# Optimization experiments

Hardware: AMD Instinct MI355X
Metric: run time of the kernel (lower is better)

The kernel has to match this reference:

```python
import jax, jax.numpy as jnp
import numpy as np

N_NODES = 50000
NODE_DIM = 256
HIDDEN = 512
N_EDGES = 500000


def setup_inputs() -> dict:
    key = jax.random.key(0)
    k1, k2, k3, k4 = jax.random.split(key, 4)
    x = jax.random.normal(k1, (N_NODES, NODE_DIM), dtype=jnp.float32)
    edge_index = jax.random.randint(k2, (2, N_EDGES), 0, N_NODES, dtype=jnp.int64)
    in_dim = 2 * NODE_DIM  # concat mode
    W1 = jax.random.normal(k3, (in_dim, HIDDEN), dtype=jnp.float32) / np.sqrt(in_dim)
    b1 = jnp.zeros((HIDDEN,), dtype=jnp.float32)
    W2 = jax.random.normal(k4, (HIDDEN, 1), dtype=jnp.float32) / np.sqrt(HIDDEN)
    b2 = jnp.zeros((1,), dtype=jnp.float32)
    return {"x": x, "edge_index": edge_index, "W1": W1, "b1": b1, "W2": W2, "b2": b2}


def reference(x, edge_index, W1, b1, W2, b2):
    row, col = edge_index[0], edge_index[1]
    # concat mode: edge_feat [E, 2*node_dim]
    edge_feat = jnp.concatenate([x[row], x[col]], axis=1)
    h = jax.nn.relu(edge_feat @ W1 + b1)  # [E, hidden]
    score = (h @ W2 + b2).squeeze(-1)     # [E]
    return score
```

## Files before the change

### kernel.cpp

```cpp
#include <hip/hip_runtime.h>
#include <hip/hip_bf16.h>

#define N_NODES  50000
#define NODE_DIM 256
#define HIDDEN   512
#define N_EDGES  500000
#define M_PAD    50048
#define NCAT     1024
#define KDIM     256
#define NB       391
#define CAP      1536
#define NSLOTS   (NB * CAP)
#define QSCALE   30.238095f
#define DSCALE   0.033070866f
#define DUMMY    0xFFFFFFFF00000000ULL

typedef __attribute__((ext_vector_type(4))) unsigned short ushort4v;
typedef __attribute__((ext_vector_type(8))) __bf16 bf16x8;
typedef __attribute__((ext_vector_type(4))) float f32x4;
typedef __attribute__((ext_vector_type(4))) unsigned int uint4v;
typedef __attribute__((ext_vector_type(2))) unsigned int uint2v;
typedef __attribute__((ext_vector_type(2))) unsigned long long ull2;
typedef __attribute__((ext_vector_type(2))) float float2v;

__device__ __forceinline__ unsigned short f2bf(float f) {
  unsigned int u = __builtin_bit_cast(unsigned int, f);
  u += 0x7fffu + ((u >> 16) & 1u);
  return (unsigned short)(u >> 16);
}

__device__ __forceinline__ void gload16(const void* g, void* l) {
  __builtin_amdgcn_global_load_lds(
      (__attribute__((address_space(1))) void*)(g),
      (__attribute__((address_space(3))) void*)(l),
      16, 0, 0);
}

__global__ void prep_kernel(const float* __restrict__ x, unsigned short* __restrict__ xb,
                            const float* __restrict__ W1, unsigned short* __restrict__ wt,
                            int* __restrict__ counts, unsigned long long* __restrict__ slots) {
  const int b = blockIdx.x;
  if (b < 2048) {
    const int total4 = M_PAD * NODE_DIM / 4;
    const int valid4 = N_NODES * NODE_DIM / 4;
    for (int i = b * 256 + threadIdx.x; i < total4; i += 2048 * 256) {
      ushort4v o;
      if (i < valid4) {
        float4 v = ((const float4*)x)[i];
        o[0] = f2bf(v.x); o[1] = f2bf(v.y); o[2] = f2bf(v.z); o[3] = f2bf(v.w);
      } else {
        o[0] = 0; o[1] = 0; o[2] = 0; o[3] = 0;
      }
      ((ushort4v*)xb)[i] = o;
    }
  } else if (b < 3072) {
    int i = (b - 2048) * 256 + threadIdx.x;
    int n = i >> 8;
    int k = i & 255;
    int srow = (n >= HIDDEN) ? (NODE_DIM + k) : k;
    int scol = n & (HIDDEN - 1);
    wt[i] = f2bf(W1[srow * HIDDEN + scol]);
  } else if (b == 3072) {
    for (int i = threadIdx.x; i < NB; i += 256) counts[i] = 0;
  } else {
    int bb = b - 3073;
    for (int i = bb * 256 + threadIdx.x; i < NSLOTS; i += 512 * 256)
      slots[i] = DUMMY;
  }
}

__global__ __launch_bounds__(256, 2) void gemm_kernel(
    const unsigned short* __restrict__ Xb,
    const unsigned short* __restrict__ Wt,
    const float* __restrict__ b1,
    unsigned short* __restrict__ CbA,
    signed char* __restrict__ CbB) {
  __shared__ unsigned short As[128 * 32];
  __shared__ unsigned short Bs[128 * 32];
  const int t = threadIdx.x;
  const int w = t >> 6;
  const int lane = t & 63;
  const int bid = blockIdx.x;
  const int xcd = bid & 7;
  const int loc = bid >> 3;
  const int tileN = loc / 49;
  const int tileM = xcd * 49 + (loc - tileN * 49);
  if (tileM >= 391) return;
  const int wm = w >> 1, wn = w & 1;

  f32x4 acc[4][4] = {};

  const int rowA0 = tileM * 128;
  const int rowB0 = tileN * 128;
  const int rstage = t >> 2;
  const int cstage = (t & 3) * 8;

  for (int kk = 0; kk < KDIM; kk += 32) {
#pragma unroll
    for (int i = 0; i < 2; ++i) {
      const unsigned short* srcA = Xb + (size_t)(rowA0 + i * 64 + rstage) * KDIM + kk + cstage;
      gload16(srcA, (char*)As + i * 4096 + w * 1024);
      const unsigned short* srcB = Wt + (size_t)(rowB0 + i * 64 + rstage) * KDIM + kk + cstage;
      gload16(srcB, (char*)Bs + i * 4096 + w * 1024);
    }
    __syncthreads();

    bf16x8 a[4], bfr[4];
#pragma unroll
    for (int fm = 0; fm < 4; ++fm)
      a[fm] = *(const bf16x8*)&As[(wm * 64 + fm * 16 + (lane & 15)) * 32 + (lane >> 4) * 8];
#pragma unroll
    for (int fn = 0; fn < 4; ++fn)
      bfr[fn] = *(const bf16x8*)&Bs[(wn * 64 + fn * 16 + (lane & 15)) * 32 + (lane >> 4) * 8];
#pragma unroll
    for (int fm = 0; fm < 4; ++fm)
#pragma unroll
      for (int fn = 0; fn < 4; ++fn)
        acc[fm][fn] = __builtin_amdgcn_mfma_f32_16x16x32_bf16(a[fm], bfr[fn], acc[fm][fn], 0, 0, 0);
    __syncthreads();
  }

  const int row0 = tileM * 128 + wm * 64;
  if (tileN < 4) {
    const int col0 = tileN * 128 + wn * 64;
    float b1v[4];
#pragma unroll
    for (int fn = 0; fn < 4; ++fn) b1v[fn] = b1[col0 + fn * 16 + (lane & 15)];
#pragma unroll
    for (int fm = 0; fm < 4; ++fm)
#pragma unroll
      for (int fn = 0; fn < 4; ++fn)
#pragma unroll
        for (int r = 0; r < 4; ++r) {
          int row = row0 + fm * 16 + (lane >> 4) * 4 + r;
          int col = col0 + fn * 16 + (lane & 15);
          CbA[(size_t)row * HIDDEN + col] = f2bf(acc[fm][fn][r] + b1v[fn]);
        }
  } else {
    const int col0 = (tileN - 4) * 128 + wn * 64;
#pragma unroll
    for (int fm = 0; fm < 4; ++fm)
#pragma unroll
      for (int fn = 0; fn < 4; ++fn)
#pragma unroll
        for (int r = 0; r < 4; ++r) {
          int row = row0 + fm * 16 + (lane >> 4) * 4 + r;
          int col = col0 + fn * 16 + (lane & 15);
          float v = fminf(fmaxf(acc[fm][fn][r], -4.2f), 4.2f);
          CbB[(size_t)row * HIDDEN + col] = (signed char)__float2int_rn(v * QSCALE);
        }
  }
}

__global__ void scatter_kernel(const int* __restrict__ ei, int* __restrict__ counts,
                               unsigned long long* __restrict__ slots) {
  __shared__ int h[NB];
  __shared__ int bbase[NB];
  const int chunk = (N_EDGES + gridDim.x - 1) / gridDim.x;
  const int e0 = blockIdx.x * chunk;
  const int e1 = min(e0 + chunk, N_EDGES);
  for (int i = threadIdx.x; i < NB; i += blockDim.x) h[i] = 0;
  __syncthreads();
  for (int e = e0 + threadIdx.x; e < e1; e += blockDim.x)
    atomicAdd(&h[ei[e] >> 7], 1);
  __syncthreads();
  for (int i = threadIdx.x; i < NB; i += blockDim.x) {
    int c = h[i];
    bbase[i] = c ? atomicAdd(&counts[i], c) : 0;
    h[i] = 0;
  }
  __syncthreads();
  for (int e = e0 + threadIdx.x; e < e1; e += blockDim.x) {
    int r = ei[e];
    int c = ei[N_EDGES + e];
    int b = r >> 7;
    int idx = bbase[b] + atomicAdd(&h[b], 1);
    slots[(size_t)b * CAP + idx] =
        (unsigned long long)r | ((unsigned long long)c << 16) | ((unsigned long long)e << 32);
  }
}

__device__ __forceinline__ float2v edge_mlp_pk(uint4v ua, uint2v ub,
                                               const float2v* w2p) {
  const float2v dscale2 = {DSCALE, DSCALE};
  const float2v zero2 = {0.f, 0.f};
  float2v acc = zero2;
#pragma unroll
  for (int j = 0; j < 4; ++j) {
    unsigned int au = ua[j];
    float2v a;
    a[0] = __builtin_bit_cast(float, au << 16);
    a[1] = __builtin_bit_cast(float, au & 0xffff0000u);
    unsigned int ubw = ub[j >> 1];
    int sh = (j & 1) * 16;
    float2v q;
    q[0] = (float)(int)(signed char)(ubw >> sh);
    q[1] = (float)(int)(signed char)(ubw >> (sh + 8));
    float2v h = __builtin_elementwise_fma(q, dscale2, a);
    h = __builtin_elementwise_max(h, zero2);
    acc = __builtin_elementwise_fma(h, w2p[j], acc);
  }
  return acc;
}

__global__ __launch_bounds__(256) void edge_kernel(
    const unsigned short* __restrict__ CbA,
    const signed char* __restrict__ CbB,
    const unsigned long long* __restrict__ slots,
    const float* __restrict__ W2,
    const float* __restrict__ b2,
    float* __restrict__ out) {
  const int lane = threadIdx.x & 63;
  const int xcd = blockIdx.x & 7;
  const int lwid = (blockIdx.x >> 3) * 4 + (threadIdx.x >> 6);
  const int nlw = (gridDim.x >> 3) * 4;
  const int per_xcd = NSLOTS / 8;
  const int pbase = xcd * per_xcd;
  const int base = lane * 8;

  float2v w2p[4];
  {
    float4 u0 = *(const float4*)&W2[base];
    float4 u1 = *(const float4*)&W2[base + 4];
    w2p[0] = (float2v){u0.x, u0.y};
    w2p[1] = (float2v){u0.z, u0.w};
    w2p[2] = (float2v){u1.x, u1.y};
    w2p[3] = (float2v){u1.z, u1.w};
  }
  const float bias2 = b2[0];

  const int pend = pbase + per_xcd;
  for (int p = pbase + lwid * 2; p < pend; p += nlw * 2) {
    ull2 rr = *(const ull2*)(slots + p);
    const int id0 = (int)(rr[0] >> 32);
    const int id1 = (int)(rr[1] >> 32);
    if ((id0 & id1) < 0) continue;
    const int r0 = (int)(rr[0] & 0xFFFF), c0 = (int)((rr[0] >> 16) & 0xFFFF);
    const int r1 = (int)(rr[1] & 0xFFFF), c1 = (int)((rr[1] >> 16) & 0xFFFF);
    uint4v ua0 = *(const uint4v*)(CbA + (size_t)r0 * HIDDEN + base);
    uint2v ub0 = *(const uint2v*)(CbB + (size_t)c0 * HIDDEN + base);
    uint4v ua1 = *(const uint4v*)(CbA + (size_t)r1 * HIDDEN + base);
    uint2v ub1 = *(const uint2v*)(CbB + (size_t)c1 * HIDDEN + base);

    float2v a0 = edge_mlp_pk(ua0, ub0, w2p);
    float2v a1 = edge_mlp_pk(ua1, ub1, w2p);
    float acc0 = a0[0] + a0[1];
    float acc1 = a1[0] + a1[1];
#pragma unroll
    for (int off = 32; off; off >>= 1) {
      acc0 += __shfl_xor(acc0, off, 64);
      acc1 += __shfl_xor(acc1, off, 64);
    }
    if (lane == 0) {
      if (id0 >= 0) out[id0] = acc0 + bias2;
      if (id1 >= 0) out[id1] = acc1 + bias2;
    }
  }
}

extern "C" void kernel_launch(void* const* d_in, const int* in_sizes, int n_in,
                              void* d_out, int out_size, void* d_ws, size_t ws_size,
                              hipStream_t stream) {
  const float* x  = (const float*)d_in[0];
  const int*   ei = (const int*)d_in[1];
  const float* W1 = (const float*)d_in[2];
  const float* b1 = (const float*)d_in[3];
  const float* W2 = (const float*)d_in[4];
  const float* b2 = (const float*)d_in[5];
  float* out = (float*)d_out;

  char* ws = (char*)d_ws;
  const size_t xb_bytes  = (size_t)M_PAD * KDIM * 2;
  const size_t wt_bytes  = (size_t)NCAT * KDIM * 2;
  const size_t cbA_bytes = (size_t)M_PAD * HIDDEN * 2;
  const size_t cbB_bytes = (size_t)M_PAD * HIDDEN;
  unsigned short* xb  = (unsigned short*)ws;
  unsigned short* wt  = (unsigned short*)(ws + xb_bytes);
  unsigned short* cbA = (unsigned short*)(ws + xb_bytes + wt_bytes);
  signed char*    cbB = (signed char*)(ws + xb_bytes + wt_bytes + cbA_bytes);
  char* tail = ws + xb_bytes + wt_bytes + cbA_bytes + cbB_bytes;
  int* counts = (int*)tail;
  unsigned long long* slots = (unsigned long long*)(tail + 4096);

  hipLaunchKernelGGL(prep_kernel, dim3(3585), dim3(256), 0, stream, x, xb, W1, wt, counts, slots);
  hipLaunchKernelGGL(gemm_kernel, dim3(392 * 8), dim3(256), 0, stream,
                     xb, wt, b1, cbA, cbB);
  hipLaunchKernelGGL(scatter_kernel, dim3(512), dim3(256), 0, stream, ei, counts, slots);
  hipLaunchKernelGGL(edge_kernel, dim3(2048), dim3(256), 0, stream, cbA, cbB, slots, W2, b2, out);
}
```

Baseline: 151.8 us.

## Replace bucketed edge slots with per-row CSR sort and row-reuse edge loop

Replaces the coarse 128-row bucket slots (padded with dummy records) with an exact CSR layout built from a per-source-node histogram, a three-kernel prefix scan, and an atomic-cursor scatter. The edge kernel now iterates over source rows, loading and unpacking each row's CbA slice once and reusing it for all of that row's edges, so only CbB is gathered per edge. This removes the dummy-slot fill and per-edge CbA gathers, but adds four small kernel launches and per-node global atomics. Per-row work is uneven, which may cause load imbalance across waves.

```diff
diff --git a/kernel.cpp b/kernel.cpp
--- a/kernel.cpp
+++ b/kernel.cpp
@@ -8,19 +8,15 @@
 #define M_PAD    50048
 #define NCAT     1024
 #define KDIM     256
-#define NB       391
-#define CAP      1536
-#define NSLOTS   (NB * CAP)
+#define NROWF    50176
 #define QSCALE   30.238095f
 #define DSCALE   0.033070866f
-#define DUMMY    0xFFFFFFFF00000000ULL
 
 typedef __attribute__((ext_vector_type(4))) unsigned short ushort4v;
 typedef __attribute__((ext_vector_type(8))) __bf16 bf16x8;
 typedef __attribute__((ext_vector_type(4))) float f32x4;
 typedef __attribute__((ext_vector_type(4))) unsigned int uint4v;
 typedef __attribute__((ext_vector_type(2))) unsigned int uint2v;
-typedef __attribute__((ext_vector_type(2))) unsigned long long ull2;
 typedef __attribute__((ext_vector_type(2))) float float2v;
 
 __device__ __forceinline__ unsigned short f2bf(float f) {
@@ -38,7 +34,7 @@
 
 __global__ void prep_kernel(const float* __restrict__ x, unsigned short* __restrict__ xb,
                             const float* __restrict__ W1, unsigned short* __restrict__ wt,
-                            int* __restrict__ counts, unsigned long long* __restrict__ slots) {
+                            int* __restrict__ hist) {
   const int b = blockIdx.x;
   if (b < 2048) {
     const int total4 = M_PAD * NODE_DIM / 4;
@@ -60,12 +56,9 @@
     int srow = (n >= HIDDEN) ? (NODE_DIM + k) : k;
     int scol = n & (HIDDEN - 1);
     wt[i] = f2bf(W1[srow * HIDDEN + scol]);
-  } else if (b == 3072) {
-    for (int i = threadIdx.x; i < NB; i += 256) counts[i] = 0;
   } else {
-    int bb = b - 3073;
-    for (int i = bb * 256 + threadIdx.x; i < NSLOTS; i += 512 * 256)
-      slots[i] = DUMMY;
+    for (int i = (b - 3072) * 256 + threadIdx.x; i < NROWF; i += 513 * 256)
+      hist[i] = 0;
   }
 }
 
@@ -152,70 +145,81 @@
   }
 }
 
-__global__ void scatter_kernel(const int* __restrict__ ei, int* __restrict__ counts,
-                               unsigned long long* __restrict__ slots) {
-  __shared__ int h[NB];
-  __shared__ int bbase[NB];
-  const int chunk = (N_EDGES + gridDim.x - 1) / gridDim.x;
-  const int e0 = blockIdx.x * chunk;
-  const int e1 = min(e0 + chunk, N_EDGES);
-  for (int i = threadIdx.x; i < NB; i += blockDim.x) h[i] = 0;
+__global__ void hist_kernel(const int* __restrict__ ei, int* __restrict__ hist) {
+  for (int e = blockIdx.x * 256 + threadIdx.x; e < N_EDGES; e += gridDim.x * 256)
+    atomicAdd(&hist[ei[e]], 1);
+}
+
+__global__ void scanA_kernel(const int* __restrict__ hist, int* __restrict__ psum) {
+  __shared__ int s[256];
+  const int t = threadIdx.x;
+  s[t] = hist[blockIdx.x * 256 + t];
   __syncthreads();
-  for (int e = e0 + threadIdx.x; e < e1; e += blockDim.x)
-    atomicAdd(&h[ei[e] >> 7], 1);
+  for (int o = 128; o; o >>= 1) {
+    if (t < o) s[t] += s[t + o];
+    __syncthreads();
+  }
+  if (t == 0) psum[blockIdx.x] = s[0];
+}
+
+__global__ void scanB_kernel(const int* __restrict__ psum, int* __restrict__ pbase) {
+  __shared__ int s[256];
+  const int t = threadIdx.x;
+  int v = (t < 196) ? psum[t] : 0;
+  s[t] = v;
   __syncthreads();
-  for (int i = threadIdx.x; i < NB; i += blockDim.x) {
-    int c = h[i];
-    bbase[i] = c ? atomicAdd(&counts[i], c) : 0;
-    h[i] = 0;
-  }
+  for (int o = 1; o < 256; o <<= 1) {
+    int u = (t >= o) ? s[t - o] : 0;
+    __syncthreads();
+    s[t] += u;
+    __syncthreads();
+  }
+  if (t < 196) pbase[t] = s[t] - v;
+}
+
+__global__ void scanC_kernel(const int* __restrict__ hist, const int* __restrict__ pbase,
+                             int* __restrict__ offs, int* __restrict__ cursor) {
+  __shared__ int s[256];
+  const int t = threadIdx.x;
+  const int idx = blockIdx.x * 256 + t;
+  int v = hist[idx];
+  s[t] = v;
   __syncthreads();
-  for (int e = e0 + threadIdx.x; e < e1; e += blockDim.x) {
+  for (int o = 1; o < 256; o <<= 1) {
+    int u = (t >= o) ? s[t - o] : 0;
+    __syncthreads();
+    s[t] += u;
+    __syncthreads();
+  }
+  int off = pbase[blockIdx.x] + s[t] - v;
+  offs[idx] = off;
+  cursor[idx] = off;
+}
+
+__global__ void scatter_kernel(const int* __restrict__ ei, int* __restrict__ cursor,
+                               unsigned long long* __restrict__ recs) {
+  for (int e = blockIdx.x * 256 + threadIdx.x; e < N_EDGES; e += gridDim.x * 256) {
     int r = ei[e];
     int c = ei[N_EDGES + e];
-    int b = r >> 7;
-    int idx = bbase[b] + atomicAdd(&h[b], 1);
-    slots[(size_t)b * CAP + idx] =
-        (unsigned long long)r | ((unsigned long long)c << 16) | ((unsigned long long)e << 32);
-  }
-}
-
-__device__ __forceinline__ float2v edge_mlp_pk(uint4v ua, uint2v ub,
-                                               const float2v* w2p) {
-  const float2v dscale2 = {DSCALE, DSCALE};
-  const float2v zero2 = {0.f, 0.f};
-  float2v acc = zero2;
-#pragma unroll
-  for (int j = 0; j < 4; ++j) {
-    unsigned int au = ua[j];
-    float2v a;
-    a[0] = __builtin_bit_cast(float, au << 16);
-    a[1] = __builtin_bit_cast(float, au & 0xffff0000u);
-    unsigned int ubw = ub[j >> 1];
-    int sh = (j & 1) * 16;
-    float2v q;
-    q[0] = (float)(int)(signed char)(ubw >> sh);
-    q[1] = (float)(int)(signed char)(ubw >> (sh + 8));
-    float2v h = __builtin_elementwise_fma(q, dscale2, a);
-    h = __builtin_elementwise_max(h, zero2);
-    acc = __builtin_elementwise_fma(h, w2p[j], acc);
-  }
-  return acc;
+    int pos = atomicAdd(&cursor[r], 1);
+    recs[pos] = (unsigned long long)(unsigned int)c | ((unsigned long long)e << 32);
+  }
 }
 
 __global__ __launch_bounds__(256) void edge_kernel(
     const unsigned short* __restrict__ CbA,
     const signed char* __restrict__ CbB,
-    const unsigned long long* __restrict__ slots,
+    const int* __restrict__ offs,
+    const unsigned long long* __restrict__ recs,
     const float* __restrict__ W2,
     const float* __restrict__ b2,
     float* __restrict__ out) {
   const int lane = threadIdx.x & 63;
   const int xcd = blockIdx.x & 7;
-  const int lwid = (blockIdx.x >> 3) * 4 + (threadIdx.x >> 6);
+  const int lw = (blockIdx.x >> 3) * 4 + (threadIdx.x >> 6);
   const int nlw = (gridDim.x >> 3) * 4;
-  const int per_xcd = NSLOTS / 8;
-  const int pbase = xcd * per_xcd;
+  const int ROWS_X = NROWF / 8;
+  const int rbase = xcd * ROWS_X;
   const int base = lane * 8;
 
   float2v w2p[4];
@@ -228,32 +232,84 @@
     w2p[3] = (float2v){u1.z, u1.w};
   }
   const float bias2 = b2[0];
-
-  const int pend = pbase + per_xcd;
-  for (int p = pbase + lwid * 2; p < pend; p += nlw * 2) {
-    ull2 rr = *(const ull2*)(slots + p);
-    const int id0 = (int)(rr[0] >> 32);
-    const int id1 = (int)(rr[1] >> 32);
-    if ((id0 & id1) < 0) continue;
-    const int r0 = (int)(rr[0] & 0xFFFF), c0 = (int)((rr[0] >> 16) & 0xFFFF);
-    const int r1 = (int)(rr[1] & 0xFFFF), c1 = (int)((rr[1] >> 16) & 0xFFFF);
-    uint4v ua0 = *(const uint4v*)(CbA + (size_t)r0 * HIDDEN + base);
-    uint2v ub0 = *(const uint2v*)(CbB + (size_t)c0 * HIDDEN + base);
-    uint4v ua1 = *(const uint4v*)(CbA + (size_t)r1 * HIDDEN + base);
-    uint2v ub1 = *(const uint2v*)(CbB + (size_t)c1 * HIDDEN + base);
-
-    float2v a0 = edge_mlp_pk(ua0, ub0, w2p);
-    float2v a1 = edge_mlp_pk(ua1, ub1, w2p);
-    float acc0 = a0[0] + a0[1];
-    float acc1 = a1[0] + a1[1];
-#pragma unroll
-    for (int off = 32; off; off >>= 1) {
-      acc0 += __shfl_xor(acc0, off, 64);
-      acc1 += __shfl_xor(acc1, off, 64);
-    }
-    if (lane == 0) {
-      if (id0 >= 0) out[id0] = acc0 + bias2;
-      if (id1 >= 0) out[id1] = acc1 + bias2;
+  const float2v dscale2 = {DSCALE, DSCALE};
+  const float2v zero2 = {0.f, 0.f};
+
+  for (int r = rbase + lw; r < rbase + ROWS_X; r += nlw) {
+    if (r >= N_NODES) continue;
+    const int off0 = offs[r];
+    const int off1 = offs[r + 1];
+    if (off0 == off1) continue;
+
+    uint4v ua = *(const uint4v*)(CbA + (size_t)r * HIDDEN + base);
+    float2v a[4];
+#pragma unroll
+    for (int j = 0; j < 4; ++j) {
+      a[j][0] = __builtin_bit_cast(float, ua[j] << 16);
+      a[j][1] = __builtin_bit_cast(float, ua[j] & 0xffff0000u);
+    }
+
+    int e = off0;
+    for (; e + 1 < off1; e += 2) {
+      unsigned long long rec0 = recs[e];
+      unsigned long long rec1 = recs[e + 1];
+      const int c0 = (int)(unsigned int)rec0;
+      const int c1 = (int)(unsigned int)rec1;
+      const int id0 = (int)(rec0 >> 32);
+      const int id1 = (int)(rec1 >> 32);
+      uint2v ub0 = *(const uint2v*)(CbB + (size_t)c0 * HIDDEN + base);
+      uint2v ub1 = *(const uint2v*)(CbB + (size_t)c1 * HIDDEN + base);
+      float2v acc0v = zero2, acc1v = zero2;
+#pragma unroll
+      for (int j = 0; j < 4; ++j) {
+        unsigned int uw0 = ub0[j >> 1], uw1 = ub1[j >> 1];
+        int sh = (j & 1) * 16;
+        float2v q0, q1;
+        q0[0] = (float)(int)(signed char)(uw0 >> sh);
+        q0[1] = (float)(int)(signed char)(uw0 >> (sh + 8));
+        q1[0] = (float)(int)(signed char)(uw1 >> sh);
+        q1[1] = (float)(int)(signed char)(uw1 >> (sh + 8));
+        float2v h0 = __builtin_elementwise_fma(q0, dscale2, a[j]);
+        float2v h1 = __builtin_elementwise_fma(q1, dscale2, a[j]);
+        h0 = __builtin_elementwise_max(h0, zero2);
+        h1 = __builtin_elementwise_max(h1, zero2);
+        acc0v = __builtin_elementwise_fma(h0, w2p[j], acc0v);
+        acc1v = __builtin_elementwise_fma(h1, w2p[j], acc1v);
+      }
+      float acc0 = acc0v[0] + acc0v[1];
+      float acc1 = acc1v[0] + acc1v[1];
+#pragma unroll
+      for (int off = 32; off; off >>= 1) {
+        acc0 += __shfl_xor(acc0, off, 64);
+        acc1 += __shfl_xor(acc1, off, 64);
+      }
+      if (lane == 0) {
+        out[id0] = acc0 + bias2;
+        out[id1] = acc1 + bias2;
+      }
+    }
+    if (e < off1) {
+      unsigned long long rec0 = recs[e];
+      const int c0 = (int)(unsigned int)rec0;
+      const int id0 = (int)(rec0 >> 32);
+      uint2v ub0 = *(const uint2v*)(CbB + (size_t)c0 * HIDDEN + base);
+      float2v acc0v = zero2;
+#pragma unroll
+      for (int j = 0; j < 4; ++j) {
+        unsigned int uw0 = ub0[j >> 1];
+        int sh = (j & 1) * 16;
+        float2v q0;
+        q0[0] = (float)(int)(signed char)(uw0 >> sh);
+        q0[1] = (float)(int)(signed char)(uw0 >> (sh + 8));
+        float2v h0 = __builtin_elementwise_fma(q0, dscale2, a[j]);
+        h0 = __builtin_elementwise_max(h0, zero2);
+        acc0v = __builtin_elementwise_fma(h0, w2p[j], acc0v);
+      }
+      float acc0 = acc0v[0] + acc0v[1];
+#pragma unroll
+      for (int off = 32; off; off >>= 1)
+        acc0 += __shfl_xor(acc0, off, 64);
+      if (lane == 0) out[id0] = acc0 + bias2;
     }
   }
 }
@@ -279,12 +335,21 @@
   unsigned short* cbA = (unsigned short*)(ws + xb_bytes + wt_bytes);
   signed char*    cbB = (signed char*)(ws + xb_bytes + wt_bytes + cbA_bytes);
   char* tail = ws + xb_bytes + wt_bytes + cbA_bytes + cbB_bytes;
-  int* counts = (int*)tail;
-  unsigned long long* slots = (unsigned long long*)(tail + 4096);
-
-  hipLaunchKernelGGL(prep_kernel, dim3(3585), dim3(256), 0, stream, x, xb, W1, wt, counts, slots);
+  int* hist   = (int*)tail;
+  int* offs   = (int*)(tail + 4 * (size_t)NROWF);
+  int* cursor = (int*)(tail + 8 * (size_t)NROWF);
+  int* psum   = (int*)(tail + 12 * (size_t)NROWF);
+  int* pbase  = (int*)(tail + 12 * (size_t)NROWF + 1024);
+  unsigned long long* recs = (unsigned long long*)(tail + 12 * (size_t)NROWF + 4096);
+
+  hipLaunchKernelGGL(prep_kernel, dim3(3585), dim3(256), 0, stream, x, xb, W1, wt, hist);
   hipLaunchKernelGGL(gemm_kernel, dim3(392 * 8), dim3(256), 0, stream,
                      xb, wt, b1, cbA, cbB);
-  hipLaunchKernelGGL(scatter_kernel, dim3(512), dim3(256), 0, stream, ei, counts, slots);
-  hipLaunchKernelGGL(edge_kernel, dim3(2048), dim3(256), 0, stream, cbA, cbB, slots, W2, b2, out);
-}
+  hipLaunchKernelGGL(hist_kernel, dim3(512), dim3(256), 0, stream, ei, hist);
+  hipLaunchKernelGGL(scanA_kernel, dim3(NROWF / 256), dim3(256), 0, stream, hist, psum);
+  hipLaunchKernelGGL(scanB_kernel, dim3(1), dim3(256), 0, stream, psum, pbase);
+  hipLaunchKernelGGL(scanC_kernel, dim3(NROWF / 256), dim3(256), 0, stream, hist, pbase, offs, cursor);
+  hipLaunchKernelGGL(scatter_kernel, dim3(512), dim3(256), 0, stream, ei, cursor, recs);
+  hipLaunchKernelGGL(edge_kernel, dim3(2048), dim3(256), 0, stream,
+                     cbA, cbB, offs, recs, W2, b2, out);
+}
```

Measured after the change: 195.3 us. 1.29x slower.
